# Kernel tuning notes

Measured on AMD Instinct MI355X. Metric: run time of the kernel, lower is better.

The kernel has to match this reference:

```python
import jax, jax.numpy as jnp
import numpy as np

EPS = 1e-5

def _conv3x3(x, w, stride=1):
    # x: [N,C,H,W], w: [O,I,3,3], padding=1
    return jax.lax.conv_general_dilated(
        x, w,
        window_strides=(stride, stride),
        padding=((1, 1), (1, 1)),
        dimension_numbers=("NCHW", "OIHW", "NCHW"),
    )

def _bn(x, gamma, beta, mean, var):
    # inference-mode BatchNorm2d with running stats; per-channel over C of NCHW
    inv = gamma * jax.lax.rsqrt(var + EPS)
    return x * inv[None, :, None, None] + (beta - mean * inv)[None, :, None, None]

def setup_inputs() -> dict:
    key = jax.random.key(0)
    ks = jax.random.split(key, 11)
    N, C, H, W = 32, 256, 56, 56
    x = jax.random.normal(ks[0], (N, C, H, W), dtype=jnp.float32)
    fan = C * 9
    w1 = jax.random.normal(ks[1], (C, C, 3, 3), dtype=jnp.float32) / np.sqrt(fan)
    w2 = jax.random.normal(ks[2], (C, C, 3, 3), dtype=jnp.float32) / np.sqrt(fan)
    g1 = jax.random.uniform(ks[3], (C,), dtype=jnp.float32, minval=0.5, maxval=1.5)
    b1 = jax.random.normal(ks[4], (C,), dtype=jnp.float32) * 0.1
    m1 = jax.random.normal(ks[5], (C,), dtype=jnp.float32) * 0.1
    v1 = jax.random.uniform(ks[6], (C,), dtype=jnp.float32, minval=0.5, maxval=1.5)
    g2 = jax.random.uniform(ks[7], (C,), dtype=jnp.float32, minval=0.5, maxval=1.5)
    b2 = jax.random.normal(ks[8], (C,), dtype=jnp.float32) * 0.1
    m2 = jax.random.normal(ks[9], (C,), dtype=jnp.float32) * 0.1
    v2 = jax.random.uniform(ks[10], (C,), dtype=jnp.float32, minval=0.5, maxval=1.5)
    return {"x": x, "w1": w1, "g1": g1, "b1": b1, "m1": m1, "v1": v1,
            "w2": w2, "g2": g2, "b2": b2, "m2": m2, "v2": v2}

def reference(x, w1, g1, b1, m1, v1, w2, g2, b2, m2, v2):
    identity = x
    out = jax.nn.relu(_bn(_conv3x3(x, w1, stride=1), g1, b1, m1, v1))
    out = _bn(_conv3x3(out, w2, stride=1), g2, b2, m2, v2)
    return jax.nn.relu(out + identity)
```

## Files before the change

### kernel.cpp

```cpp
#include <hip/hip_runtime.h>
#include <hip/hip_bf16.h>


typedef __attribute__((ext_vector_type(8))) short bf16x8;
typedef __attribute__((ext_vector_type(4))) float f32x4;
typedef __attribute__((ext_vector_type(4))) unsigned int uint4v;

#define C_CH   256
#define HW_IMG 3136
#define CHW    802816
#define WELEM  589824
#define RSTR   40
#define BUFE   7680
#define NCH    8
#define ZROW   15360

__device__ __forceinline__ ushort f2bf(float f){
    union{__hip_bfloat16 h; ushort u;} c; c.h = __float2bfloat16(f); return c.u;
}

__global__ __launch_bounds__(256) void prep_kernel(
    const float* __restrict__ w1, const float* __restrict__ w2,
    const float* __restrict__ g1, const float* __restrict__ b1,
    const float* __restrict__ m1, const float* __restrict__ v1,
    const float* __restrict__ g2, const float* __restrict__ b2,
    const float* __restrict__ m2, const float* __restrict__ v2,
    ushort* __restrict__ wf1, ushort* __restrict__ wf2,
    float* __restrict__ bn, ushort* __restrict__ zb)
{
    int gid = blockIdx.x * 256 + threadIdx.x;
    if (gid < WELEM) {
        int j = gid & 7, l = (gid >> 3) & 63, ct = (gid >> 9) & 15, rr = gid >> 13;
        int c = rr / 9, r = rr - c * 9;
        int co = ct * 16 + (l & 15);
        int ci = c * 32 + (l >> 4) * 8 + j;
        wf1[gid] = f2bf(w1[(co * C_CH + ci) * 9 + r]);
    }
    int g2i = gid - WELEM;
    if (g2i >= 0 && g2i < WELEM) {
        int j = g2i & 7, l = (g2i >> 3) & 63, ct = (g2i >> 9) & 15, rr = g2i >> 13;
        int c = rr / 9, r = rr - c * 9;
        int co = ct * 16 + (l & 15);
        int ci = c * 32 + (l >> 4) * 8 + j;
        wf2[g2i] = f2bf(w2[(co * C_CH + ci) * 9 + r]);
    }
    if (gid < C_CH) {
        float i1 = g1[gid] * rsqrtf(v1[gid] + 1e-5f);
        bn[gid]            = i1;
        bn[C_CH + gid]     = b1[gid] - m1[gid] * i1;
        float i2 = g2[gid] * rsqrtf(v2[gid] + 1e-5f);
        bn[2*C_CH + gid]   = i2;
        bn[3*C_CH + gid]   = b2[gid] - m2[gid] * i2;
    }
    if (gid < 512) zb[gid] = 0;
}

__global__ __launch_bounds__(256) void xpose_kernel(
    const float* __restrict__ x, ushort* __restrict__ xT)
{
    __shared__ ushort T[64 * 72];
    int tid = threadIdx.x;
    int b = blockIdx.x;
    int n = b / 196, rem = b % 196;
    int pb = rem >> 2, cb = rem & 3;
    int lane = tid & 63, cr = tid >> 6;
    const float* xp = x + ((size_t)(n * C_CH + cb * 64)) * HW_IMG + pb * 64 + lane;
#pragma unroll
    for (int j = 0; j < 16; ++j) {
        int cil = cr * 16 + j;
        T[lane * 72 + cil] = f2bf(xp[(size_t)cil * HW_IMG]);
    }
    __syncthreads();
#pragma unroll
    for (int it = 0; it < 2; ++it) {
        int slot = it * 256 + tid;
        int p = slot >> 3, g = slot & 7;
        uint4v v = *(const uint4v*)&T[p * 72 + g * 8];
        *(uint4v*)(xT + ((size_t)n * HW_IMG + pb * 64 + p) * C_CH + cb * 64 + g * 8) = v;
    }
}

#define READB(dst, bufE, s)                                                  \
    {                                                                        \
        const int dw_ = (s) % 3 - 1;                                         \
        const int off_ = ((s) / 3 - 1) * 56 * RSTR + dw_ * RSTR + (bufE);    \
        _Pragma("unroll")                                                    \
        for (int nc_ = 0; nc_ < 4; ++nc_) {                                  \
            bool ok_ = (dw_ == -1) ? wLa[nc_]                                \
                                   : ((dw_ == 1) ? wRa[nc_] : true);         \
            int idx_ = ok_ ? (vbe[nc_] + off_) : zidx;                       \
            dst[nc_] = *(const bf16x8*)&B[idx_];                             \
        }                                                                    \
    }

#define MFMA16(bq, t)                                                        \
    __builtin_amdgcn_s_setprio(1);                                           \
    _Pragma("unroll")                                                        \
    for (int mr_ = 0; mr_ < 4; ++mr_) {                                      \
        _Pragma("unroll")                                                    \
        for (int nc_ = 0; nc_ < 4; ++nc_)                                    \
            acc[mr_][nc_] = __builtin_amdgcn_mfma_f32_16x16x32_bf16(         \
                areg[(t) % 3][mr_], bq[nc_], acc[mr_][nc_], 0, 0, 0);        \
    }                                                                        \
    __builtin_amdgcn_s_setprio(0);

#define LOADA(toff, slot)                                                    \
    {                                                                        \
        _Pragma("unroll")                                                    \
        for (int mr_ = 0; mr_ < 4; ++mr_)                                    \
            areg[slot][mr_] = *(const bf16x8*)(pW + (toff) * 8192 + mr_ * 512);\
    }

template<bool SECOND>
__global__ __launch_bounds__(256, 2) void conv_kernel(
    const ushort* __restrict__ srcT,
    const ushort* __restrict__ wf,
    const float* __restrict__ bnp,
    const float* __restrict__ ident,
    const ushort* __restrict__ zb,
    void* __restrict__ dst)
{
    __shared__ ushort B[16896];

    const int tid = threadIdx.x;
    const int wv = tid >> 6, l = tid & 63;
    const int lr = l & 15, lg = l >> 4;

    int bid = blockIdx.x;
    int swz = (bid & 7) * 196 + (bid >> 3);
    const int n = swz / 49, pt = swz % 49;
    const int p0 = pt * 64;

    bool wLa[4], wRa[4];
    int vbe[4];
#pragma unroll
    for (int nc = 0; nc < 4; ++nc) {
        int p = p0 + nc * 16 + lr;
        int w = p % 56;
        wLa[nc] = (w > 0);
        wRa[nc] = (w < 55);
        vbe[nc] = (64 + nc * 16 + lr) * RSTR + lg * 8;
    }
    const int zidx = ZROW + lg * 8;

    const ushort* sA[4];
#pragma unroll
    for (int rd = 0; rd < 4; ++rd) {
        int slot = rd * 256 + tid;
        int row = slot / 5, g = slot - row * 5;
        int gp = p0 - 64 + row;
        bool val = (g < 4) && (gp >= 0) && (gp < HW_IMG) && (slot < 960);
        sA[rd] = val ? (srcT + ((size_t)n * HW_IMG + gp) * C_CH + g * 8)
                     : (zb + g * 8);
    }

    auto stage = [&](int cix, int bufE) {
#pragma unroll
        for (int rd = 0; rd < 4; ++rd) {
            if (rd < 3 || tid < 192) {
                __builtin_amdgcn_global_load_lds(
                    (const __attribute__((address_space(1))) void*)(sA[rd] + cix * 32),
                    (__attribute__((address_space(3))) void*)&B[bufE + (rd * 256 + tid) * 8],
                    16, 0, 0);
            }
        }
    };

    f32x4 acc[4][4];
#pragma unroll
    for (int mr = 0; mr < 4; ++mr)
#pragma unroll
        for (int nc = 0; nc < 4; ++nc) {
            f32x4 z = {0.f, 0.f, 0.f, 0.f};
            acc[mr][nc] = z;
        }

    bf16x8 areg[3][4];
    const ushort* pW = wf + wv * 2048 + l * 8;

    stage(0, 0);
    if (tid < 40) B[ZROW + tid] = 0;
    LOADA(0, 0);
    LOADA(1, 1);
    __syncthreads();

#pragma unroll 1
    for (int c2 = 0; c2 < 4; ++c2) {
        {
            bf16x8 bqA[4], bqB[4];
            READB(bqA, 0, 0);
#pragma unroll
            for (int s = 0; s < 9; ++s) {
                LOADA(s + 2, (s + 2) % 3);
                if (s == 3) stage(2 * c2 + 1, BUFE);
                if ((s & 1) == 0) {
                    if (s + 1 < 9) READB(bqB, 0, s + 1);
                    MFMA16(bqA, s);
                } else {
                    READB(bqA, 0, s + 1);
                    MFMA16(bqB, s);
                }
            }
        }
        __syncthreads();
        {
            bf16x8 bqA[4], bqB[4];
            READB(bqA, BUFE, 0);
#pragma unroll
            for (int s = 0; s < 9; ++s) {
                const int t = s + 9;
                if (s < 7 || c2 < 3) LOADA(t + 2, (t + 2) % 3);
                if (s == 3 && c2 < 3) stage(2 * c2 + 2, 0);
                if ((s & 1) == 0) {
                    if (s + 1 < 9) READB(bqB, BUFE, s + 1);
                    MFMA16(bqA, t);
                } else {
                    READB(bqA, BUFE, s + 1);
                    MFMA16(bqB, t);
                }
            }
        }
        __syncthreads();
        pW += 18 * 8192;
    }

    if constexpr (!SECOND) {
        ushort* T = B;
#pragma unroll
        for (int mr = 0; mr < 4; ++mr) {
#pragma unroll
            for (int nc = 0; nc < 4; ++nc) {
                int co0 = wv * 64 + mr * 16 + lg * 4;
                float v0 = fmaxf(acc[mr][nc][0] * bnp[co0+0] + bnp[C_CH+co0+0], 0.f);
                float v1 = fmaxf(acc[mr][nc][1] * bnp[co0+1] + bnp[C_CH+co0+1], 0.f);
                float v2 = fmaxf(acc[mr][nc][2] * bnp[co0+2] + bnp[C_CH+co0+2], 0.f);
                float v3 = fmaxf(acc[mr][nc][3] * bnp[co0+3] + bnp[C_CH+co0+3], 0.f);
                uint2 pk;
                pk.x = (uint)f2bf(v0) | ((uint)f2bf(v1) << 16);
                pk.y = (uint)f2bf(v2) | ((uint)f2bf(v3) << 16);
                *(uint2*)&T[(nc * 16 + lr) * 264 + co0] = pk;
            }
        }
        __syncthreads();
        ushort* yT = (ushort*)dst;
#pragma unroll
        for (int it = 0; it < 8; ++it) {
            int slot = it * 256 + tid;
            int row = slot >> 5, g = slot & 31;
            uint4v v = *(const uint4v*)&T[row * 264 + g * 8];
            *(uint4v*)(yT + ((size_t)n * HW_IMG + p0 + row) * C_CH + g * 8) = v;
        }
    } else {
        const size_t nbase = (size_t)n * CHW;
        float* out = (float*)dst;
#pragma unroll
        for (int mr = 0; mr < 4; ++mr) {
#pragma unroll
            for (int nc = 0; nc < 4; ++nc) {
                int pc = p0 + nc * 16 + lr;
#pragma unroll
                for (int i = 0; i < 4; ++i) {
                    int co = wv * 64 + mr * 16 + lg * 4 + i;
                    size_t o = nbase + (size_t)co * HW_IMG + pc;
                    float val = acc[mr][nc][i] * bnp[co] + bnp[C_CH + co] + ident[o];
                    out[o] = fmaxf(val, 0.f);
                }
            }
        }
    }
}

extern "C" void kernel_launch(void* const* d_in, const int* in_sizes, int n_in,
                              void* d_out, int out_size, void* d_ws, size_t ws_size,
                              hipStream_t stream) {
    const float* x  = (const float*)d_in[0];
    const float* w1 = (const float*)d_in[1];
    const float* g1 = (const float*)d_in[2];
    const float* b1 = (const float*)d_in[3];
    const float* m1 = (const float*)d_in[4];
    const float* v1 = (const float*)d_in[5];
    const float* w2 = (const float*)d_in[6];
    const float* g2 = (const float*)d_in[7];
    const float* b2 = (const float*)d_in[8];
    const float* m2 = (const float*)d_in[9];
    const float* v2 = (const float*)d_in[10];

    ushort* wf1 = (ushort*)d_ws;
    ushort* wf2 = wf1 + WELEM;
    float*  bn  = (float*)(wf2 + WELEM);
    ushort* zb  = (ushort*)(bn + 4 * C_CH);
    ushort* yT  = zb + 512;
    ushort* xT  = (ushort*)d_out;

    prep_kernel<<<dim3(4608), dim3(256), 0, stream>>>(
        w1, w2, g1, b1, m1, v1, g2, b2, m2, v2, wf1, wf2, bn, zb);

    xpose_kernel<<<dim3(6272), dim3(256), 0, stream>>>(x, xT);

    conv_kernel<false><<<dim3(1568), dim3(256), 0, stream>>>(
        xT, wf1, bn, x, zb, (void*)yT);

    conv_kernel<true><<<dim3(1568), dim3(256), 0, stream>>>(
        yT, wf2, bn + 512, x, zb, d_out);
}
```

Baseline: 257.5 us.

## Read conv B operands directly from global memory instead of staging in LDS

The conv kernel no longer stages the input halo tile into shared memory with global_load_lds double buffering. Each lane now loads its bf16x8 B fragments straight from the transposed NHWC global tensor, using per-lane row and column boundary masks that point at a zero buffer placed just past the tensor. This removes the LDS staging and the block barriers inside the main loop, but relies on L1/L2 caching to absorb the nine-fold reuse of each input element across taps. It also adds global-load latency to the MFMA pipeline.

Result: slower. 586.8 us (+127.9%).

```diff
diff --git a/kernel.cpp b/kernel.cpp
--- a/kernel.cpp
+++ b/kernel.cpp
@@ -10,10 +10,7 @@
 #define HW_IMG 3136
 #define CHW    802816
 #define WELEM  589824
-#define RSTR   40
-#define BUFE   7680
-#define NCH    8
-#define ZROW   15360
+#define ZBELEM 25690112
 
 __device__ __forceinline__ ushort f2bf(float f){
     union{__hip_bfloat16 h; ushort u;} c; c.h = __float2bfloat16(f); return c.u;
@@ -26,7 +23,7 @@
     const float* __restrict__ g2, const float* __restrict__ b2,
     const float* __restrict__ m2, const float* __restrict__ v2,
     ushort* __restrict__ wf1, ushort* __restrict__ wf2,
-    float* __restrict__ bn, ushort* __restrict__ zb)
+    float* __restrict__ bn, ushort* __restrict__ xzb, ushort* __restrict__ yzb)
 {
     int gid = blockIdx.x * 256 + threadIdx.x;
     if (gid < WELEM) {
@@ -52,7 +49,7 @@
         bn[2*C_CH + gid]   = i2;
         bn[3*C_CH + gid]   = b2[gid] - m2[gid] * i2;
     }
-    if (gid < 512) zb[gid] = 0;
+    if (gid < 512) { xzb[gid] = 0; yzb[gid] = 0; }
 }
 
 __global__ __launch_bounds__(256) void xpose_kernel(
@@ -80,27 +77,27 @@
     }
 }
 
-#define READB(dst, bufE, s)                                                  \
+#define READB_G(dstq, s, cbytes)                                             \
     {                                                                        \
-        const int dw_ = (s) % 3 - 1;                                         \
-        const int off_ = ((s) / 3 - 1) * 56 * RSTR + dw_ * RSTR + (bufE);    \
+        const int dh_ = (s) / 3 - 1, dw_ = (s) % 3 - 1;                      \
+        const int off_ = (dh_ * 56 + dw_) * 512;                  \
         _Pragma("unroll")                                                    \
         for (int nc_ = 0; nc_ < 4; ++nc_) {                                  \
-            bool ok_ = (dw_ == -1) ? wLa[nc_]                                \
-                                   : ((dw_ == 1) ? wRa[nc_] : true);         \
-            int idx_ = ok_ ? (vbe[nc_] + off_) : zidx;                       \
-            dst[nc_] = *(const bf16x8*)&B[idx_];                             \
+            bool ok_ = ((dh_ == -1) ? hU[nc_] : (dh_ == 1) ? hD[nc_] : true) \
+                    && ((dw_ == -1) ? wL[nc_] : (dw_ == 1) ? wR[nc_] : true);\
+            uint vo_ = ok_ ? (vb[nc_] + (uint)off_ + (cbytes)) : zo;         \
+            dstq[nc_] = *(const bf16x8*)(sIb + vo_);                         \
         }                                                                    \
     }
 
-#define MFMA16(bq, t)                                                        \
+#define MFMA16(bq, s)                                                        \
     __builtin_amdgcn_s_setprio(1);                                           \
     _Pragma("unroll")                                                        \
     for (int mr_ = 0; mr_ < 4; ++mr_) {                                      \
         _Pragma("unroll")                                                    \
         for (int nc_ = 0; nc_ < 4; ++nc_)                                    \
             acc[mr_][nc_] = __builtin_amdgcn_mfma_f32_16x16x32_bf16(         \
-                areg[(t) % 3][mr_], bq[nc_], acc[mr_][nc_], 0, 0, 0);        \
+                areg[(s) % 3][mr_], bq[nc_], acc[mr_][nc_], 0, 0, 0);        \
     }                                                                        \
     __builtin_amdgcn_s_setprio(0);
 
@@ -117,10 +114,9 @@
     const ushort* __restrict__ wf,
     const float* __restrict__ bnp,
     const float* __restrict__ ident,
-    const ushort* __restrict__ zb,
     void* __restrict__ dst)
 {
-    __shared__ ushort B[16896];
+    __shared__ ushort T[16896];
 
     const int tid = threadIdx.x;
     const int wv = tid >> 6, l = tid & 63;
@@ -131,40 +127,20 @@
     const int n = swz / 49, pt = swz % 49;
     const int p0 = pt * 64;
 
-    bool wLa[4], wRa[4];
-    int vbe[4];
+    bool wL[4], wR[4], hU[4], hD[4];
+    uint vb[4];
 #pragma unroll
     for (int nc = 0; nc < 4; ++nc) {
         int p = p0 + nc * 16 + lr;
         int w = p % 56;
-        wLa[nc] = (w > 0);
-        wRa[nc] = (w < 55);
-        vbe[nc] = (64 + nc * 16 + lr) * RSTR + lg * 8;
-    }
-    const int zidx = ZROW + lg * 8;
-
-    const ushort* sA[4];
-#pragma unroll
-    for (int rd = 0; rd < 4; ++rd) {
-        int slot = rd * 256 + tid;
-        int row = slot / 5, g = slot - row * 5;
-        int gp = p0 - 64 + row;
-        bool val = (g < 4) && (gp >= 0) && (gp < HW_IMG) && (slot < 960);
-        sA[rd] = val ? (srcT + ((size_t)n * HW_IMG + gp) * C_CH + g * 8)
-                     : (zb + g * 8);
-    }
-
-    auto stage = [&](int cix, int bufE) {
-#pragma unroll
-        for (int rd = 0; rd < 4; ++rd) {
-            if (rd < 3 || tid < 192) {
-                __builtin_amdgcn_global_load_lds(
-                    (const __attribute__((address_space(1))) void*)(sA[rd] + cix * 32),
-                    (__attribute__((address_space(3))) void*)&B[bufE + (rd * 256 + tid) * 8],
-                    16, 0, 0);
-            }
-        }
-    };
+        wL[nc] = (w > 0);
+        wR[nc] = (w < 55);
+        hU[nc] = (p >= 56);
+        hD[nc] = (p < HW_IMG - 56);
+        vb[nc] = (uint)(p * 512 + lg * 16);
+    }
+    const char* sIb = (const char*)(srcT + (size_t)n * HW_IMG * C_CH);
+    const uint  zo  = (uint)((size_t)(32 - n) * HW_IMG * 512) + (uint)(lg * 16);
 
     f32x4 acc[4][4];
 #pragma unroll
@@ -176,56 +152,34 @@
         }
 
     bf16x8 areg[3][4];
-    const ushort* pW = wf + wv * 2048 + l * 8;
-
-    stage(0, 0);
-    if (tid < 40) B[ZROW + tid] = 0;
-    LOADA(0, 0);
-    LOADA(1, 1);
-    __syncthreads();
+    const ushort* pW0 = wf + wv * 2048 + l * 8;
+
+    {
+        const ushort* pW = pW0;
+        LOADA(0, 0);
+        LOADA(1, 1);
+    }
 
 #pragma unroll 1
-    for (int c2 = 0; c2 < 4; ++c2) {
-        {
-            bf16x8 bqA[4], bqB[4];
-            READB(bqA, 0, 0);
-#pragma unroll
-            for (int s = 0; s < 9; ++s) {
-                LOADA(s + 2, (s + 2) % 3);
-                if (s == 3) stage(2 * c2 + 1, BUFE);
-                if ((s & 1) == 0) {
-                    if (s + 1 < 9) READB(bqB, 0, s + 1);
-                    MFMA16(bqA, s);
-                } else {
-                    READB(bqA, 0, s + 1);
-                    MFMA16(bqB, s);
-                }
+    for (int c = 0; c < 8; ++c) {
+        const uint cbytes = (uint)(c * 64);
+        const ushort* pW = pW0 + (size_t)c * 9 * 8192;
+        bf16x8 bqA[4], bqB[4];
+        READB_G(bqA, 0, cbytes);
+#pragma unroll
+        for (int s = 0; s < 9; ++s) {
+            if (s < 7 || c < 7) LOADA(s + 2, (s + 2) % 3);
+            if ((s & 1) == 0) {
+                if (s + 1 < 9) READB_G(bqB, s + 1, cbytes);
+                MFMA16(bqA, s);
+            } else {
+                READB_G(bqA, s + 1, cbytes);
+                MFMA16(bqB, s);
             }
         }
-        __syncthreads();
-        {
-            bf16x8 bqA[4], bqB[4];
-            READB(bqA, BUFE, 0);
-#pragma unroll
-            for (int s = 0; s < 9; ++s) {
-                const int t = s + 9;
-                if (s < 7 || c2 < 3) LOADA(t + 2, (t + 2) % 3);
-                if (s == 3 && c2 < 3) stage(2 * c2 + 2, 0);
-                if ((s & 1) == 0) {
-                    if (s + 1 < 9) READB(bqB, BUFE, s + 1);
-                    MFMA16(bqA, t);
-                } else {
-                    READB(bqA, BUFE, s + 1);
-                    MFMA16(bqB, t);
-                }
-            }
-        }
-        __syncthreads();
-        pW += 18 * 8192;
     }
 
     if constexpr (!SECOND) {
-        ushort* T = B;
 #pragma unroll
         for (int mr = 0; mr < 4; ++mr) {
 #pragma unroll
@@ -288,18 +242,18 @@
     ushort* wf1 = (ushort*)d_ws;
     ushort* wf2 = wf1 + WELEM;
     float*  bn  = (float*)(wf2 + WELEM);
-    ushort* zb  = (ushort*)(bn + 4 * C_CH);
-    ushort* yT  = zb + 512;
+    ushort* yT  = (ushort*)(bn + 4 * C_CH);
     ushort* xT  = (ushort*)d_out;
 
     prep_kernel<<<dim3(4608), dim3(256), 0, stream>>>(
-        w1, w2, g1, b1, m1, v1, g2, b2, m2, v2, wf1, wf2, bn, zb);
+        w1, w2, g1, b1, m1, v1, g2, b2, m2, v2, wf1, wf2, bn,
+        xT + ZBELEM, yT + ZBELEM);
 
     xpose_kernel<<<dim3(6272), dim3(256), 0, stream>>>(x, xT);
 
     conv_kernel<false><<<dim3(1568), dim3(256), 0, stream>>>(
-        xT, wf1, bn, x, zb, (void*)yT);
+        xT, wf1, bn, x, (void*)yT);
 
     conv_kernel<true><<<dim3(1568), dim3(256), 0, stream>>>(
-        yT, wf2, bn + 512, x, zb, d_out);
-}
+        yT, wf2, bn + 512, x, d_out);
+}
```
